# Optimization experiments

Measured on AMD Instinct MI355X. Metric: run time of the kernel, lower is better.

## Reference

```python
import jax, jax.numpy as jnp
import numpy as np
from jax import lax

K = 5          # dynamic kernel size
GROUPS = 8     # inter_channels // group_channels = 128 // 16
R = 2          # pixel shuffle upscale factor
SLOPE = 0.01   # LeakyReLU default negative_slope
EPS = 1e-5     # BatchNorm eps


def conv2d(x, w, b, pad=0):
    # x: [B,C,H,W], w: [O,I,kh,kw]
    y = lax.conv_general_dilated(x, w, (1, 1), [(pad, pad), (pad, pad)],
                                 dimension_numbers=('NCHW', 'OIHW', 'NCHW'))
    return y + b[None, :, None, None]


def pixel_shuffle(x, r):
    B, C, H, W = x.shape
    x = x.reshape(B, C // (r * r), r, r, H, W)
    x = x.transpose(0, 1, 4, 2, 5, 3)  # B, C', H, r, W, r
    return x.reshape(B, C // (r * r), H * r, W * r)


def involution(x, weight, k, groups, pad):
    # x: [B,C,H,W]; weight: [B,groups,k,k,H,W]
    # out[b, g*gc+c, h, w] = sum_ij weight[b,g,i,j,h,w] * x_pad[b, g*gc+c, h+i, w+j]
    B, C, H, W = x.shape
    gc = C // groups
    xp = jnp.pad(x, ((0, 0), (0, 0), (pad, pad), (pad, pad)))
    xg = xp.reshape(B, groups, gc, H + 2 * pad, W + 2 * pad)
    out = jnp.zeros((B, groups, gc, H, W), x.dtype)
    for i in range(k):
        for j in range(k):
            out = out + weight[:, :, None, i, j] * xg[:, :, :, i:i + H, j:j + W]
    return out.reshape(B, C, H, W)


def setup_inputs() -> dict:
    key = jax.random.key(0)
    ks = jax.random.split(key, 16)
    s = 0.05
    return {
        'high_level': jax.random.normal(ks[0], (8, 128, 64, 64), jnp.float32),
        'low_level': jax.random.normal(ks[1], (8, 224, 128, 128), jnp.float32),
        'emb': jax.random.normal(ks[2], (8, 256, 128, 128), jnp.float32),
        'reduce_w': jax.random.normal(ks[3], (128, 256, 1, 1), jnp.float32) * s,
        'reduce_b': jax.random.normal(ks[4], (128,), jnp.float32) * s,
        'conv1_w': jax.random.normal(ks[5], (32, 128, 1, 1), jnp.float32) * s,
        'conv1_b': jax.random.normal(ks[6], (32,), jnp.float32) * s,
        'conv2_w': jax.random.normal(ks[7], (200, 32, 3, 3), jnp.float32) * s,
        'conv2_b': jax.random.normal(ks[8], (200,), jnp.float32) * s,
        'embconv_w': jax.random.normal(ks[9], (32, 256, 1, 1), jnp.float32) * s,
        'embconv_b': jax.random.normal(ks[10], (32,), jnp.float32) * s,
        'out_w': jax.random.normal(ks[11], (64, 128, 1, 1), jnp.float32) * s,
        'out_b': jax.random.normal(ks[12], (64,), jnp.float32) * s,
        'bn_gamma': jnp.ones((64,), jnp.float32),
        'bn_beta': jnp.zeros((64,), jnp.float32),
        'bn_mean': jnp.zeros((64,), jnp.float32),
        'bn_var': jax.random.uniform(ks[13], (64,), jnp.float32, 0.5, 1.5),
    }


def reference(high_level, low_level, emb,
              reduce_w, reduce_b, conv1_w, conv1_b, conv2_w, conv2_b,
              embconv_w, embconv_b, out_w, out_b,
              bn_gamma, bn_beta, bn_mean, bn_var):
    cat = jnp.concatenate([pixel_shuffle(high_level, R), low_level], axis=1)
    cat = conv2d(cat, reduce_w, reduce_b)
    mix = jax.nn.leaky_relu(conv2d(cat, conv1_w, conv1_b)
                            + conv2d(emb, embconv_w, embconv_b), SLOPE)
    w = conv2d(mix, conv2_w, conv2_b, pad=1)  # [B, K*K*GROUPS, H, W]
    B, _, H, W = w.shape
    w = w.reshape(B, GROUPS, K, K, H, W)
    o = involution(cat, w, K, GROUPS, (K - 1) // 2)
    o = conv2d(o, out_w, out_b)
    o = (o - bn_mean[None, :, None, None]) * (bn_gamma[None, :, None, None]
        / jnp.sqrt(bn_var[None, :, None, None] + EPS)) + bn_beta[None, :, None, None]
    return jax.nn.leaky_relu(o, SLOPE)
```

## Files before the change

kernel.cpp:

```cpp
#include <hip/hip_runtime.h>

typedef unsigned short u16; typedef unsigned int u32; typedef unsigned long long u64;
typedef __attribute__((ext_vector_type(8))) short short8;
typedef __attribute__((ext_vector_type(16))) float f32x16;

#define HW 16384

#define RED_B  0
#define C1E_B  128
#define C2_B   160
#define OUT_B  416
#define BN_SC  480
#define BN_SH  544
#define FLAG_OFF   4096
#define RWB_OFF    8192
#define C1B_OFF    73728
#define EMBB_OFF   81920
#define OUTB_OFF   98304
#define C2PB_OFF   114688
#define CAT2_OFF   524288
#define MIX_OFF    34078720

__device__ __forceinline__ float bf2f(u16 x){ u32 u=((u32)x)<<16; float f; __builtin_memcpy(&f,&u,4); return f; }
__device__ __forceinline__ u16 f2bf(float f){ u32 u; __builtin_memcpy(&u,&f,4); return (u16)((u + 0x7fffu + ((u>>16)&1u))>>16); }
__device__ __forceinline__ float lrelu(float x){ return x>0.f ? x : 0.01f*x; }

template<int M> __device__ __forceinline__ u16 ldb(const void* p, size_t i){
    if (M==1) return ((const u16*)p)[i];
    return f2bf(((const float*)p)[i]);
}
template<int M> __device__ __forceinline__ float ldf(const void* p, size_t i){
    if (M==1) return bf2f(((const u16*)p)[i]);
    return ((const float*)p)[i];
}
template<int M> __device__ __forceinline__ short8 ld8(const void* p, size_t i){
    short8 v;
    if (M==1){ __builtin_memcpy(&v, (const u16*)p + i, 16); }
    else {
        float a[8]; __builtin_memcpy(a, (const float*)p + i, 32);
#pragma unroll
        for (int r=0;r<8;r++) v[r] = (short)f2bf(a[r]);
    }
    return v;
}
template<int M> __device__ __forceinline__ void ld4(const void* p, size_t i, u32* d){
    if (M==1){ __builtin_memcpy(d, (const u16*)p + i, 8); }
    else {
        float a[4]; __builtin_memcpy(a, (const float*)p + i, 16);
        d[0] = (u32)f2bf(a[0]) | ((u32)f2bf(a[1])<<16);
        d[1] = (u32)f2bf(a[2]) | ((u32)f2bf(a[3])<<16);
    }
}
__device__ __forceinline__ int swz(int p){ return ((p>>1) ^ (p>>3)) & 7; }

__global__ void detect_kernel(const void* __restrict__ emb, u32* __restrict__ flag){
    int tid = threadIdx.x;
    const u16* p = (const u16*)emb;
    int e = (p[tid*2] >> 7) & 0xFF;
    u64 m = __ballot(e >= 100 && e <= 140);
    if (tid == 0) *flag = (__popcll(m) >= 32) ? 1u : 0u;
}

template<int M>
__device__ __forceinline__ void prep_body(
    const void* rw, const void* rb, const void* c1w, const void* c1b,
    const void* c2w, const void* c2b, const void* ew, const void* eb,
    const void* ow, const void* ob, const void* gam, const void* bet,
    const void* mn, const void* vr, char* ws)
{
    float* wf = (float*)ws;
    int i = blockIdx.x*256 + threadIdx.x;
    if (i < 32768) {
        int o = i>>8, ic = i&255;
        int s = ic>>4, qq = (ic>>3)&1, e = ic&7;
        int dst = (((o>>5)*16 + s)*64 + qq*32 + (o&31))*8 + e;
        ((u16*)(ws+RWB_OFF))[dst] = ldb<M>(rw, i);
    }
    else if (i < 36864)  ((u16*)(ws+C1B_OFF))[i-32768] = ldb<M>(c1w, i-32768);
    else if (i < 45056)  ((u16*)(ws+EMBB_OFF))[i-36864] = ldb<M>(ew, i-36864);
    else if (i < 53248)  ((u16*)(ws+OUTB_OFF))[i-45056] = ldb<M>(ow, i-45056);
    else if (i < 126976) {
        int j = i-53248; int o = j/288, k = j - o*288;
        int tap = k>>5, ic = k&31;
        u16 v = 0;
        if (o < 200) v = ldb<M>(c2w, (size_t)o*288 + ic*9 + tap);
        ((u16*)(ws+C2PB_OFF))[j] = v;
    }
    else if (i < 127584) {
        int j = i-126976;
        if (j < 128) wf[RED_B+j] = ldf<M>(rb, j);
        else if (j < 160) wf[C1E_B+j-128] = ldf<M>(c1b, j-128) + ldf<M>(eb, j-128);
        else if (j < 416) { int o = j-160; wf[C2_B+o] = (o<200) ? ldf<M>(c2b,o) : 0.f; }
        else if (j < 480) wf[OUT_B+j-416] = ldf<M>(ob, j-416);
        else if (j < 544) { int c=j-480; wf[BN_SC+c] = ldf<M>(gam,c) * rsqrtf(ldf<M>(vr,c)+1e-5f); }
        else { int c=j-544; wf[BN_SH+c] = ldf<M>(bet,c) - ldf<M>(mn,c)*ldf<M>(gam,c)*rsqrtf(ldf<M>(vr,c)+1e-5f); }
    }
}

__global__ __launch_bounds__(256) void k_prep(
    const void* rw, const void* rb, const void* c1w, const void* c1b,
    const void* c2w, const void* c2b, const void* ew, const void* eb,
    const void* ow, const void* ob, const void* gam, const void* bet,
    const void* mn, const void* vr, char* ws, const u32* __restrict__ flag)
{
    if (*flag) prep_body<1>(rw,rb,c1w,c1b,c2w,c2b,ew,eb,ow,ob,gam,bet,mn,vr,ws);
    else       prep_body<0>(rw,rb,c1w,c1b,c2w,c2b,ew,eb,ow,ob,gam,bet,mn,vr,ws);
}

template<int M>
__device__ __forceinline__ void reduce_body(
    const void* __restrict__ hi, const void* __restrict__ lo,
    const u16* __restrict__ rwB, const float* __restrict__ wf,
    u16* __restrict__ cat2, u16* At)
{
    const int tid = threadIdx.x, wvi = tid>>6, lane = tid&63;
    const int rt = (wvi>>1)*32, nc0 = (wvi&1)*64;
    const int col = lane&31, q = lane>>5;

    const int gpx = blockIdx.x*64;
    const int b = gpx>>14, p0 = gpx&16383;
    const int h = p0>>7, w0 = p0&127;

    const int co = tid>>3, po = tid&7;
    u32 W[8][4];
    if (co < 28) {
        u32 R[8][4];
#pragma unroll
        for (int j=0;j<8;j++){
            short8 v = ld8<M>(lo, ((size_t)(b*224 + 8*co + j))*HW + p0 + 8*po);
            __builtin_memcpy(&R[j][0], &v, 16);
        }
#pragma unroll
        for (int p=0;p<8;p++){
            const int u = p>>1, hf = p&1;
#pragma unroll
            for (int m=0;m<4;m++){
                u32 A0 = R[2*m][u], A1 = R[2*m+1][u];
                W[p][m] = hf ? ((A0>>16) | (A1 & 0xffff0000u))
                             : ((A0 & 0xffffu) | (A1<<16));
            }
        }
        const int ch = co + 4;
#pragma unroll
        for (int p=0;p<8;p++){
            int pg = 8*po + p;
            __builtin_memcpy(At + pg*264 + ((ch ^ swz(pg))<<3), &W[p][0], 16);
        }
    } else {
        const int cc0 = (co-28)*8, h2 = (h&1)*2;
        u32 E[8][2], O[8][2];
#pragma unroll
        for (int j=0;j<8;j++){
            int hc = (cc0+j)*4 + h2;
            size_t src = ((size_t)(b*128 + hc))*4096 + (size_t)(h>>1)*64 + (w0>>1) + 4*po;
            ld4<M>(hi, src,        E[j]);
            ld4<M>(hi, src + 4096, O[j]);
        }
#pragma unroll
        for (int p=0;p<8;p++){
            const int k = p>>1, u = k>>1, hf = k&1;
#pragma unroll
            for (int m=0;m<4;m++){
                u32 A0, A1;
                if (p&1){ A0 = O[2*m][u]; A1 = O[2*m+1][u]; }
                else    { A0 = E[2*m][u]; A1 = E[2*m+1][u]; }
                W[p][m] = hf ? ((A0>>16) | (A1 & 0xffff0000u))
                             : ((A0 & 0xffffu) | (A1<<16));
            }
        }
        const int ch = co - 28;
#pragma unroll
        for (int p=0;p<8;p++){
            int pg = 8*po + p;
            __builtin_memcpy(At + pg*264 + ((ch ^ swz(pg))<<3), &W[p][0], 16);
        }
    }
    __syncthreads();

    const int pp = rt + col, sw = swz(pp);
    const u16* arow = At + pp*264;
    const int ot0 = (wvi&1)*2;

    f32x16 acc0, acc1;
#pragma unroll
    for (int r=0;r<16;r++){ acc0[r]=0.f; acc1[r]=0.f; }

    short8 Bb[2][8];
#pragma unroll
    for (int nt=0;nt<2;nt++)
#pragma unroll
    for (int s=0;s<8;s++)
        __builtin_memcpy(&Bb[nt][s], rwB + (((size_t)((ot0+nt)*16 + s))*64 + lane)*8, 16);
#pragma unroll
    for (int s=0;s<8;s++){
        short8 a; __builtin_memcpy(&a, arow + (((2*s+q)^sw)<<3), 16);
        acc0 = __builtin_amdgcn_mfma_f32_32x32x16_bf16(a, Bb[0][s], acc0, 0,0,0);
        acc1 = __builtin_amdgcn_mfma_f32_32x32x16_bf16(a, Bb[1][s], acc1, 0,0,0);
    }
#pragma unroll
    for (int nt=0;nt<2;nt++)
#pragma unroll
    for (int s=0;s<8;s++)
        __builtin_memcpy(&Bb[nt][s], rwB + (((size_t)((ot0+nt)*16 + 8+s))*64 + lane)*8, 16);
#pragma unroll
    for (int s=8;s<16;s++){
        short8 a; __builtin_memcpy(&a, arow + (((2*s+q)^sw)<<3), 16);
        acc0 = __builtin_amdgcn_mfma_f32_32x32x16_bf16(a, Bb[0][s-8], acc0, 0,0,0);
        acc1 = __builtin_amdgcn_mfma_f32_32x32x16_bf16(a, Bb[1][s-8], acc1, 0,0,0);
    }

#pragma unroll
    for (int nt=0; nt<2; nt++){
        int oc = nc0 + nt*32 + col;
        float bias = wf[RED_B + oc];
#pragma unroll
        for (int r=0;r<16;r++){
            int row = (r&3) + 8*(r>>2) + 4*q;
            float v = (nt ? acc1[r] : acc0[r]) + bias;
            cat2[((size_t)(gpx + rt + row))*128 + oc] = f2bf(v);
        }
    }
}

__global__ __launch_bounds__(256) void k_reduce(
    const void* __restrict__ hi, const void* __restrict__ lo,
    const u16* __restrict__ rwB, const float* __restrict__ wf,
    u16* __restrict__ cat2, const u32* __restrict__ flag)
{
    __shared__ u16 At[64*264];
    if (*flag) reduce_body<1>(hi, lo, rwB, wf, cat2, At);
    else       reduce_body<0>(hi, lo, rwB, wf, cat2, At);
}

template<int M>
__device__ __forceinline__ void mix_body(
    const u16* __restrict__ cat2, const void* __restrict__ emb,
    const u16* __restrict__ c1B, const u16* __restrict__ embB,
    const float* __restrict__ wf, u16* __restrict__ mixt, u16* At)
{
    const int tid = threadIdx.x, wvi = tid>>6, lane = tid&63;
    const int rt = wvi*32, col = lane&31, q = lane>>5;

    const int gpx = blockIdx.x*128;
    const int b = gpx>>14, p0 = gpx&16383;

    short8 Bc[8];
#pragma unroll
    for (int s=0;s<8;s++)  __builtin_memcpy(&Bc[s], c1B + (size_t)col*128 + s*16 + q*8, 16);

    f32x16 acc;
#pragma unroll
    for (int r=0;r<16;r++) acc[r]=0.f;
    const int pp = rt + col, sw = swz(pp);
    const u16* arow = At + pp*136;

#pragma unroll
    for (int i=0;i<8;i++){
        int idx = tid + i*256;
        int p = idx>>4, c16 = idx&15;
        short8 v;
        __builtin_memcpy(&v, cat2 + ((size_t)(gpx+p))*128 + c16*8, 16);
        *(short8*)(At + p*136 + ((c16 ^ swz(p))<<3)) = v;
    }
    __syncthreads();
#pragma unroll
    for (int s=0;s<8;s++){
        short8 a; __builtin_memcpy(&a, arow + (((2*s+q)^sw)<<3), 16);
        acc = __builtin_amdgcn_mfma_f32_32x32x16_bf16(a, Bc[s], acc, 0,0,0);
    }

    const int co = tid>>4, po = tid&15;
#pragma unroll 1
    for (int half=0; half<2; half++){
        u32 R[8][4];
#pragma unroll
        for (int j=0;j<8;j++){
            short8 v = ld8<M>(emb, ((size_t)(b*256 + half*128 + 8*co + j))*HW + p0 + 8*po);
            __builtin_memcpy(&R[j][0], &v, 16);
        }
        short8 Be[8];
#pragma unroll
        for (int s=0;s<8;s++)
            __builtin_memcpy(&Be[s], embB + (size_t)col*256 + half*128 + s*16 + q*8, 16);
        __syncthreads();
        u32 W[8][4];
#pragma unroll
        for (int p=0;p<8;p++){
            const int u = p>>1, hf = p&1;
#pragma unroll
            for (int m=0;m<4;m++){
                u32 A0 = R[2*m][u], A1 = R[2*m+1][u];
                W[p][m] = hf ? ((A0>>16) | (A1 & 0xffff0000u))
                             : ((A0 & 0xffffu) | (A1<<16));
            }
        }
#pragma unroll
        for (int p=0;p<8;p++){
            int pg = 8*po + p;
            __builtin_memcpy(At + pg*136 + ((co ^ swz(pg))<<3), &W[p][0], 16);
        }
        __syncthreads();
#pragma unroll
        for (int s=0;s<8;s++){
            short8 a; __builtin_memcpy(&a, arow + (((2*s+q)^sw)<<3), 16);
            acc = __builtin_amdgcn_mfma_f32_32x32x16_bf16(a, Be[s], acc, 0,0,0);
        }
    }
    float bias = wf[C1E_B + col];
#pragma unroll
    for (int r=0;r<16;r++){
        int row = (r&3) + 8*(r>>2) + 4*q;
        mixt[((size_t)(gpx + rt + row))*32 + col] = f2bf(lrelu(acc[r] + bias));
    }
}

__global__ __launch_bounds__(256) void k_mix(
    const u16* __restrict__ cat2, const void* __restrict__ emb,
    const u16* __restrict__ c1B, const u16* __restrict__ embB,
    const float* __restrict__ wf, u16* __restrict__ mixt, const u32* __restrict__ flag)
{
    __shared__ u16 At[128*136];
    if (*flag) mix_body<1>(cat2, emb, c1B, embB, wf, mixt, At);
    else       mix_body<0>(cat2, emb, c1B, embB, wf, mixt, At);
}

template<int M>
__device__ __forceinline__ void inv_body(
    const u16* __restrict__ cat2, const u16* __restrict__ mixt,
    const u16* __restrict__ c2B, const u16* __restrict__ outB,
    const float* __restrict__ wf, void* __restrict__ out,
    u16* halo_m, u16* wgt_l, u16* halo_c, u16* og)
{
    const int tid = threadIdx.x, wvi = tid>>6, lane = tid&63;
    const int col = lane&31, q = lane>>5;
    const int b = blockIdx.y, ty = blockIdx.x>>3, tx = blockIdx.x&7;
    const int py = tid>>4, px = tid&15;

    f32x16 acc[2][2];
#pragma unroll
    for (int i=0;i<2;i++)
#pragma unroll
    for (int j=0;j<2;j++)
#pragma unroll
    for (int r=0;r<16;r++) acc[i][j][r] = 0.f;

#pragma unroll
    for (int i=0;i<6;i++){
        int idx = tid + i*256;
        if (idx < 1296){
            int point = idx>>2, cq = idx&3;
            int y = ty*16 + point/18 - 1, x = tx*16 + point%18 - 1;
            short8 v;
            if (y>=0 && y<128 && x>=0 && x<128)
                __builtin_memcpy(&v, mixt + ((size_t)(b*HW + y*128 + x))*32 + cq*8, 16);
            else { short z=0; v = (short8){z,z,z,z,z,z,z,z}; }
            *(short8*)(halo_m + point*40 + cq*8) = v;
        }
    }
    __syncthreads();

#pragma unroll 1
    for (int g=0; g<8; g++){
        __syncthreads();

        const int o = g*25 + col;
        short8 Bf[18];
#pragma unroll
        for (int s=0;s<18;s++)
            __builtin_memcpy(&Bf[s], c2B + (size_t)o*288 + s*16 + q*8, 16);

#pragma unroll
        for (int i=0;i<4;i++){
            int idx = tid + i*256;
            if (idx < 800){
                int point = idx>>1, cq = idx&1;
                int y = ty*16 + point/20 - 2, x = tx*16 + point%20 - 2;
                short8 v;
                if (y>=0 && y<128 && x>=0 && x<128)
                    __builtin_memcpy(&v, cat2 + ((size_t)(b*HW + y*128 + x))*128 + g*16 + cq*8, 16);
                else { short z=0; v = (short8){z,z,z,z,z,z,z,z}; }
                *(short8*)(halo_c + point*16 + cq*8) = v;
            }
        }

        f32x16 c0, c1;
#pragma unroll
        for (int r=0;r<16;r++){ c0[r]=0.f; c1[r]=0.f; }
        const int p0 = wvi*64 + col, p1 = p0 + 32;
        const int pya = p0>>4, pxa = p0&15, pyb = p1>>4, pxb = p1&15;
#pragma unroll
        for (int s=0;s<18;s++){
            int tap = s>>1, ih = s&1;
            int dy = tap/3, dx = tap%3;
            short8 a0, a1;
            __builtin_memcpy(&a0, halo_m + ((pya+dy)*18 + pxa+dx)*40 + ih*16 + q*8, 16);
            __builtin_memcpy(&a1, halo_m + ((pyb+dy)*18 + pxb+dx)*40 + ih*16 + q*8, 16);
            c0 = __builtin_amdgcn_mfma_f32_32x32x16_bf16(a0, Bf[s], c0, 0,0,0);
            c1 = __builtin_amdgcn_mfma_f32_32x32x16_bf16(a1, Bf[s], c1, 0,0,0);
        }
        {
            float bias = wf[C2_B + o];
#pragma unroll
            for (int rt2=0; rt2<2; rt2++){
                int mb = wvi*64 + rt2*32;
#pragma unroll
                for (int r=0;r<16;r+=2){
                    int row0 = (r&3) + 8*(r>>2) + 4*q;
                    float v0 = (rt2 ? c1[r]   : c0[r])   + bias;
                    float v1 = (rt2 ? c1[r+1] : c0[r+1]) + bias;
                    u32 pkv = (u32)f2bf(v0) | ((u32)f2bf(v1)<<16);
                    *(u32*)(wgt_l + (size_t)col*264 + mb + row0) = pkv;
                }
            }
        }
        __syncthreads();

        float wvv[25];
#pragma unroll
        for (int t=0;t<25;t++) wvv[t] = bf2f(wgt_l[t*264 + tid]);

        float a16[16];
#pragma unroll
        for (int cc=0;cc<16;cc++) a16[cc]=0.f;
#pragma unroll
        for (int t=0;t<25;t++){
            int dy = t/5, dx = t%5;
            u32 vv[8];
            __builtin_memcpy(vv, halo_c + ((py+dy)*20 + px+dx)*16, 32);
            float wt = wvv[t];
#pragma unroll
            for (int r=0;r<8;r++){
                u32 u = vv[r];
                u32 ulo = u<<16, uhi = u & 0xffff0000u;
                float x0, x1;
                __builtin_memcpy(&x0,&ulo,4); __builtin_memcpy(&x1,&uhi,4);
                a16[2*r]   += wt*x0;
                a16[2*r+1] += wt*x1;
            }
        }
        u32 pk[8];
#pragma unroll
        for (int r=0;r<8;r++) pk[r] = (u32)f2bf(a16[2*r]) | ((u32)f2bf(a16[2*r+1])<<16);
        __builtin_memcpy(og + tid*16, pk, 32);
        __syncthreads();

        short8 bo0, bo1;
        __builtin_memcpy(&bo0, outB + (size_t)(col)*128      + g*16 + q*8, 16);
        __builtin_memcpy(&bo1, outB + (size_t)(32+col)*128   + g*16 + q*8, 16);
#pragma unroll
        for (int rt2=0; rt2<2; rt2++){
            int prow = (wvi*2 + rt2)*32 + col;
            short8 a; __builtin_memcpy(&a, og + prow*16 + q*8, 16);
            acc[rt2][0] = __builtin_amdgcn_mfma_f32_32x32x16_bf16(a, bo0, acc[rt2][0], 0,0,0);
            acc[rt2][1] = __builtin_amdgcn_mfma_f32_32x32x16_bf16(a, bo1, acc[rt2][1], 0,0,0);
        }
    }
#pragma unroll
    for (int rt2=0; rt2<2; rt2++)
#pragma unroll
    for (int nt=0; nt<2; nt++){
        int oc = nt*32 + col;
        float bias = wf[OUT_B+oc], sc = wf[BN_SC+oc], sh = wf[BN_SH+oc];
#pragma unroll
        for (int r=0;r<16;r++){
            int row = (r&3) + 8*(r>>2) + 4*q;
            int p = (wvi*2 + rt2)*32 + row;
            int yy = ty*16 + (p>>4), xx = tx*16 + (p&15);
            float v = lrelu((acc[rt2][nt][r] + bias)*sc + sh);
            size_t oidx = ((size_t)(b*64 + oc))*HW + yy*128 + xx;
            if (M==1) ((u16*)out)[oidx] = f2bf(v);
            else ((float*)out)[oidx] = v;
        }
    }
}

__global__ __launch_bounds__(256,2) void k_inv(
    const u16* __restrict__ cat2, const u16* __restrict__ mixt,
    const u16* __restrict__ c2B, const u16* __restrict__ outB,
    const float* __restrict__ wf, void* __restrict__ out, const u32* __restrict__ flag)
{
    __shared__ u16 halo_m[324*40];
    __shared__ u16 wgt_l[32*264];
    __shared__ u16 halo_c[400*16];
    __shared__ u16 og[256*16];
    if (*flag) inv_body<1>(cat2, mixt, c2B, outB, wf, out, halo_m, wgt_l, halo_c, og);
    else       inv_body<0>(cat2, mixt, c2B, outB, wf, out, halo_m, wgt_l, halo_c, og);
}

extern "C" void kernel_launch(void* const* d_in, const int* in_sizes, int n_in,
                              void* d_out, int out_size, void* d_ws, size_t ws_size,
                              hipStream_t stream) {
    const void* hi  = d_in[0];
    const void* lo  = d_in[1];
    const void* emb = d_in[2];
    char* ws = (char*)d_ws;
    float* wf = (float*)ws;
    u32* flag = (u32*)(ws + FLAG_OFF);
    u16* cat2 = (u16*)(ws + CAT2_OFF);
    u16* mixt = (u16*)(ws + MIX_OFF);

    detect_kernel<<<1, 64, 0, stream>>>(emb, flag);

    k_prep<<<499,256,0,stream>>>(d_in[3],d_in[4],d_in[5],d_in[6],d_in[7],d_in[8],
        d_in[9],d_in[10],d_in[11],d_in[12],d_in[13],d_in[14],d_in[15],d_in[16], ws, flag);

    k_reduce<<<2048,256,0,stream>>>(hi, lo, (const u16*)(ws+RWB_OFF), wf, cat2, flag);

    k_mix<<<1024,256,0,stream>>>(cat2, emb, (const u16*)(ws+C1B_OFF),
                                 (const u16*)(ws+EMBB_OFF), wf, mixt, flag);

    k_inv<<<dim3(64,8),256,0,stream>>>(cat2, mixt, (const u16*)(ws+C2PB_OFF),
                                       (const u16*)(ws+OUTB_OFF), wf, d_out, flag);
}
```

Before: 399.6 us.

## Fuse reduce and mix kernels, keeping cat tile in LDS for conv1

Merges the reduce 1x1 conv kernel and the mix kernel into one kernel over 64-pixel tiles. The reduced cat tile is written to global memory for the involution stage and also kept in shared memory, so conv1 reads it from LDS instead of reloading it from global. The emb projection's K dimension is split across wave pairs, and partial sums are exchanged through LDS. This removes one launch and one global read of cat2. In exchange it uses more shared memory per block and adds a launch_bounds occupancy hint.

```diff
diff --git a/kernel.cpp b/kernel.cpp
--- a/kernel.cpp
+++ b/kernel.cpp
@@ -23,6 +23,7 @@
 
 __device__ __forceinline__ float bf2f(u16 x){ u32 u=((u32)x)<<16; float f; __builtin_memcpy(&f,&u,4); return f; }
 __device__ __forceinline__ u16 f2bf(float f){ u32 u; __builtin_memcpy(&u,&f,4); return (u16)((u + 0x7fffu + ((u>>16)&1u))>>16); }
+__device__ __forceinline__ u32 pk2(float a, float b){ return (u32)f2bf(a) | ((u32)f2bf(b)<<16); }
 __device__ __forceinline__ float lrelu(float x){ return x>0.f ? x : 0.01f*x; }
 
 template<int M> __device__ __forceinline__ u16 ldb(const void* p, size_t i){
@@ -33,25 +34,25 @@
     if (M==1) return bf2f(((const u16*)p)[i]);
     return ((const float*)p)[i];
 }
-template<int M> __device__ __forceinline__ short8 ld8(const void* p, size_t i){
-    short8 v;
-    if (M==1){ __builtin_memcpy(&v, (const u16*)p + i, 16); }
-    else {
-        float a[8]; __builtin_memcpy(a, (const float*)p + i, 32);
-#pragma unroll
-        for (int r=0;r<8;r++) v[r] = (short)f2bf(a[r]);
-    }
-    return v;
-}
-template<int M> __device__ __forceinline__ void ld4(const void* p, size_t i, u32* d){
-    if (M==1){ __builtin_memcpy(d, (const u16*)p + i, 8); }
-    else {
-        float a[4]; __builtin_memcpy(a, (const float*)p + i, 16);
-        d[0] = (u32)f2bf(a[0]) | ((u32)f2bf(a[1])<<16);
-        d[1] = (u32)f2bf(a[2]) | ((u32)f2bf(a[3])<<16);
-    }
-}
 __device__ __forceinline__ int swz(int p){ return ((p>>1) ^ (p>>3)) & 7; }
+
+template<int M>
+__device__ __forceinline__ void load8x8(const void* p, size_t base, size_t stride, u32 R[8][4]){
+    if (M==1){
+#pragma unroll
+        for (int j=0;j<8;j++)
+            __builtin_memcpy(&R[j][0], (const u16*)p + base + (size_t)j*stride, 16);
+    } else {
+        float raw[8][8];
+#pragma unroll
+        for (int j=0;j<8;j++)
+            __builtin_memcpy(&raw[j][0], (const float*)p + base + (size_t)j*stride, 32);
+#pragma unroll
+        for (int j=0;j<8;j++)
+#pragma unroll
+        for (int m=0;m<4;m++) R[j][m] = pk2(raw[j][2*m], raw[j][2*m+1]);
+    }
+}
 
 __global__ void detect_kernel(const void* __restrict__ emb, u32* __restrict__ flag){
     int tid = threadIdx.x;
@@ -108,28 +109,141 @@
 }
 
 template<int M>
-__device__ __forceinline__ void reduce_body(
-    const void* __restrict__ hi, const void* __restrict__ lo,
-    const u16* __restrict__ rwB, const float* __restrict__ wf,
-    u16* __restrict__ cat2, u16* At)
+__device__ __forceinline__ void rm_body(
+    const void* __restrict__ hi, const void* __restrict__ lo, const void* __restrict__ emb,
+    const u16* __restrict__ rwB, const u16* __restrict__ c1B, const u16* __restrict__ embB,
+    const float* __restrict__ wf, u16* __restrict__ cat2, u16* __restrict__ mixt,
+    u16* At, u16* c2l)
 {
     const int tid = threadIdx.x, wvi = tid>>6, lane = tid&63;
-    const int rt = (wvi>>1)*32, nc0 = (wvi&1)*64;
     const int col = lane&31, q = lane>>5;
-
     const int gpx = blockIdx.x*64;
     const int b = gpx>>14, p0 = gpx&16383;
     const int h = p0>>7, w0 = p0&127;
-
     const int co = tid>>3, po = tid&7;
-    u32 W[8][4];
-    if (co < 28) {
+
+    {
+        u32 W[8][4];
+        if (co < 28) {
+            u32 R[8][4];
+            load8x8<M>(lo, ((size_t)(b*224 + 8*co))*HW + p0 + 8*po, HW, R);
+#pragma unroll
+            for (int p=0;p<8;p++){
+                const int u = p>>1, hf = p&1;
+#pragma unroll
+                for (int m=0;m<4;m++){
+                    u32 A0 = R[2*m][u], A1 = R[2*m+1][u];
+                    W[p][m] = hf ? ((A0>>16) | (A1 & 0xffff0000u))
+                                 : ((A0 & 0xffffu) | (A1<<16));
+                }
+            }
+            const int ch = co + 4;
+#pragma unroll
+            for (int p=0;p<8;p++){
+                int pg = 8*po + p;
+                __builtin_memcpy(At + pg*264 + ((ch ^ swz(pg))<<3), &W[p][0], 16);
+            }
+        } else {
+            const int cc0 = (co-28)*8, h2 = (h&1)*2;
+            u32 E[8][2], O[8][2];
+            if (M==1){
+#pragma unroll
+                for (int j=0;j<8;j++){
+                    int hc = (cc0+j)*4 + h2;
+                    size_t src = ((size_t)(b*128 + hc))*4096 + (size_t)(h>>1)*64 + (w0>>1) + 4*po;
+                    __builtin_memcpy(&E[j][0], (const u16*)hi + src, 8);
+                    __builtin_memcpy(&O[j][0], (const u16*)hi + src + 4096, 8);
+                }
+            } else {
+                float rE[8][4], rO[8][4];
+#pragma unroll
+                for (int j=0;j<8;j++){
+                    int hc = (cc0+j)*4 + h2;
+                    size_t src = ((size_t)(b*128 + hc))*4096 + (size_t)(h>>1)*64 + (w0>>1) + 4*po;
+                    __builtin_memcpy(&rE[j][0], (const float*)hi + src, 16);
+                    __builtin_memcpy(&rO[j][0], (const float*)hi + src + 4096, 16);
+                }
+#pragma unroll
+                for (int j=0;j<8;j++){
+                    E[j][0] = pk2(rE[j][0], rE[j][1]); E[j][1] = pk2(rE[j][2], rE[j][3]);
+                    O[j][0] = pk2(rO[j][0], rO[j][1]); O[j][1] = pk2(rO[j][2], rO[j][3]);
+                }
+            }
+#pragma unroll
+            for (int p=0;p<8;p++){
+                const int k = p>>1, u = k>>1, hf = k&1;
+#pragma unroll
+                for (int m=0;m<4;m++){
+                    u32 A0, A1;
+                    if (p&1){ A0 = O[2*m][u]; A1 = O[2*m+1][u]; }
+                    else    { A0 = E[2*m][u]; A1 = E[2*m+1][u]; }
+                    W[p][m] = hf ? ((A0>>16) | (A1 & 0xffff0000u))
+                                 : ((A0 & 0xffffu) | (A1<<16));
+                }
+            }
+            const int ch = co - 28;
+#pragma unroll
+            for (int p=0;p<8;p++){
+                int pg = 8*po + p;
+                __builtin_memcpy(At + pg*264 + ((ch ^ swz(pg))<<3), &W[p][0], 16);
+            }
+        }
+    }
+    __syncthreads();
+
+    {
+        const int rt = (wvi>>1)*32, nc0 = (wvi&1)*64;
+        const int pp = rt + col, sw = swz(pp);
+        const u16* arow = At + pp*264;
+        const int ot0 = (wvi&1)*2;
+
+        f32x16 acc0, acc1;
+#pragma unroll
+        for (int r=0;r<16;r++){ acc0[r]=0.f; acc1[r]=0.f; }
+
+        short8 Bb[2][8];
+#pragma unroll
+        for (int nt=0;nt<2;nt++)
+#pragma unroll
+        for (int s=0;s<8;s++)
+            __builtin_memcpy(&Bb[nt][s], rwB + (((size_t)((ot0+nt)*16 + s))*64 + lane)*8, 16);
+#pragma unroll
+        for (int s=0;s<8;s++){
+            short8 a; __builtin_memcpy(&a, arow + (((2*s+q)^sw)<<3), 16);
+            acc0 = __builtin_amdgcn_mfma_f32_32x32x16_bf16(a, Bb[0][s], acc0, 0,0,0);
+            acc1 = __builtin_amdgcn_mfma_f32_32x32x16_bf16(a, Bb[1][s], acc1, 0,0,0);
+        }
+#pragma unroll
+        for (int nt=0;nt<2;nt++)
+#pragma unroll
+        for (int s=0;s<8;s++)
+            __builtin_memcpy(&Bb[nt][s], rwB + (((size_t)((ot0+nt)*16 + 8+s))*64 + lane)*8, 16);
+#pragma unroll
+        for (int s=8;s<16;s++){
+            short8 a; __builtin_memcpy(&a, arow + (((2*s+q)^sw)<<3), 16);
+            acc0 = __builtin_amdgcn_mfma_f32_32x32x16_bf16(a, Bb[0][s-8], acc0, 0,0,0);
+            acc1 = __builtin_amdgcn_mfma_f32_32x32x16_bf16(a, Bb[1][s-8], acc1, 0,0,0);
+        }
+
+#pragma unroll
+        for (int nt=0; nt<2; nt++){
+            int oc = nc0 + nt*32 + col;
+            float bias = wf[RED_B + oc];
+#pragma unroll
+            for (int r=0;r<16;r++){
+                int row = (r&3) + 8*(r>>2) + 4*q;
+                int px = rt + row;
+                u16 bv = f2bf((nt ? acc1[r] : acc0[r]) + bias);
+                cat2[((size_t)(gpx + px))*128 + oc] = bv;
+                c2l[px*136 + (((oc>>3) ^ swz(px))<<3) + (oc&7)] = bv;
+            }
+        }
+    }
+
+    {
         u32 R[8][4];
-#pragma unroll
-        for (int j=0;j<8;j++){
-            short8 v = ld8<M>(lo, ((size_t)(b*224 + 8*co + j))*HW + p0 + 8*po);
-            __builtin_memcpy(&R[j][0], &v, 16);
-        }
+        load8x8<M>(emb, ((size_t)(b*256 + 8*co))*HW + p0 + 8*po, HW, R);
+        u32 W[8][4];
 #pragma unroll
         for (int p=0;p<8;p++){
             const int u = p>>1, hf = p&1;
@@ -140,188 +254,87 @@
                              : ((A0 & 0xffffu) | (A1<<16));
             }
         }
-        const int ch = co + 4;
+        __syncthreads();
 #pragma unroll
         for (int p=0;p<8;p++){
             int pg = 8*po + p;
-            __builtin_memcpy(At + pg*264 + ((ch ^ swz(pg))<<3), &W[p][0], 16);
+            __builtin_memcpy(At + pg*264 + ((co ^ swz(pg))<<3), &W[p][0], 16);
+        }
+    }
+    __syncthreads();
+
+    const int rt2 = wvi>>1, q2 = wvi&1;
+    const int pp2 = rt2*32 + col, sw2 = swz(pp2);
+    const u16* arow136 = c2l + pp2*136;
+    const u16* arow264 = At + pp2*264;
+
+    f32x16 macc;
+#pragma unroll
+    for (int r=0;r<16;r++) macc[r]=0.f;
+
+    if (q2 == 0){
+        short8 Bc[8];
+#pragma unroll
+        for (int s=0;s<8;s++)
+            __builtin_memcpy(&Bc[s], c1B + (size_t)col*128 + s*16 + q*8, 16);
+#pragma unroll
+        for (int s=0;s<8;s++){
+            short8 a; __builtin_memcpy(&a, arow136 + (((2*s+q)^sw2)<<3), 16);
+            macc = __builtin_amdgcn_mfma_f32_32x32x16_bf16(a, Bc[s], macc, 0,0,0);
+        }
+        short8 Be[4];
+#pragma unroll
+        for (int s=0;s<4;s++)
+            __builtin_memcpy(&Be[s], embB + (size_t)col*256 + s*16 + q*8, 16);
+#pragma unroll
+        for (int s=0;s<4;s++){
+            short8 a; __builtin_memcpy(&a, arow264 + (((2*s+q)^sw2)<<3), 16);
+            macc = __builtin_amdgcn_mfma_f32_32x32x16_bf16(a, Be[s], macc, 0,0,0);
         }
     } else {
-        const int cc0 = (co-28)*8, h2 = (h&1)*2;
-        u32 E[8][2], O[8][2];
-#pragma unroll
-        for (int j=0;j<8;j++){
-            int hc = (cc0+j)*4 + h2;
-            size_t src = ((size_t)(b*128 + hc))*4096 + (size_t)(h>>1)*64 + (w0>>1) + 4*po;
-            ld4<M>(hi, src,        E[j]);
-            ld4<M>(hi, src + 4096, O[j]);
-        }
-#pragma unroll
-        for (int p=0;p<8;p++){
-            const int k = p>>1, u = k>>1, hf = k&1;
-#pragma unroll
-            for (int m=0;m<4;m++){
-                u32 A0, A1;
-                if (p&1){ A0 = O[2*m][u]; A1 = O[2*m+1][u]; }
-                else    { A0 = E[2*m][u]; A1 = E[2*m+1][u]; }
-                W[p][m] = hf ? ((A0>>16) | (A1 & 0xffff0000u))
-                             : ((A0 & 0xffffu) | (A1<<16));
-            }
-        }
-        const int ch = co - 28;
-#pragma unroll
-        for (int p=0;p<8;p++){
-            int pg = 8*po + p;
-            __builtin_memcpy(At + pg*264 + ((ch ^ swz(pg))<<3), &W[p][0], 16);
+        short8 Be[12];
+#pragma unroll
+        for (int s=0;s<12;s++)
+            __builtin_memcpy(&Be[s], embB + (size_t)col*256 + (4+s)*16 + q*8, 16);
+#pragma unroll
+        for (int s=0;s<12;s++){
+            int ks = 4 + s;
+            short8 a; __builtin_memcpy(&a, arow264 + (((2*ks+q)^sw2)<<3), 16);
+            macc = __builtin_amdgcn_mfma_f32_32x32x16_bf16(a, Be[s], macc, 0,0,0);
         }
     }
     __syncthreads();
 
-    const int pp = rt + col, sw = swz(pp);
-    const u16* arow = At + pp*264;
-    const int ot0 = (wvi&1)*2;
-
-    f32x16 acc0, acc1;
-#pragma unroll
-    for (int r=0;r<16;r++){ acc0[r]=0.f; acc1[r]=0.f; }
-
-    short8 Bb[2][8];
-#pragma unroll
-    for (int nt=0;nt<2;nt++)
-#pragma unroll
-    for (int s=0;s<8;s++)
-        __builtin_memcpy(&Bb[nt][s], rwB + (((size_t)((ot0+nt)*16 + s))*64 + lane)*8, 16);
-#pragma unroll
-    for (int s=0;s<8;s++){
-        short8 a; __builtin_memcpy(&a, arow + (((2*s+q)^sw)<<3), 16);
-        acc0 = __builtin_amdgcn_mfma_f32_32x32x16_bf16(a, Bb[0][s], acc0, 0,0,0);
-        acc1 = __builtin_amdgcn_mfma_f32_32x32x16_bf16(a, Bb[1][s], acc1, 0,0,0);
-    }
-#pragma unroll
-    for (int nt=0;nt<2;nt++)
-#pragma unroll
-    for (int s=0;s<8;s++)
-        __builtin_memcpy(&Bb[nt][s], rwB + (((size_t)((ot0+nt)*16 + 8+s))*64 + lane)*8, 16);
-#pragma unroll
-    for (int s=8;s<16;s++){
-        short8 a; __builtin_memcpy(&a, arow + (((2*s+q)^sw)<<3), 16);
-        acc0 = __builtin_amdgcn_mfma_f32_32x32x16_bf16(a, Bb[0][s-8], acc0, 0,0,0);
-        acc1 = __builtin_amdgcn_mfma_f32_32x32x16_bf16(a, Bb[1][s-8], acc1, 0,0,0);
-    }
-
-#pragma unroll
-    for (int nt=0; nt<2; nt++){
-        int oc = nc0 + nt*32 + col;
-        float bias = wf[RED_B + oc];
+    float* exch = (float*)At;
+    if (q2 == 1){
 #pragma unroll
         for (int r=0;r<16;r++){
             int row = (r&3) + 8*(r>>2) + 4*q;
-            float v = (nt ? acc1[r] : acc0[r]) + bias;
-            cat2[((size_t)(gpx + rt + row))*128 + oc] = f2bf(v);
-        }
-    }
-}
-
-__global__ __launch_bounds__(256) void k_reduce(
-    const void* __restrict__ hi, const void* __restrict__ lo,
-    const u16* __restrict__ rwB, const float* __restrict__ wf,
-    u16* __restrict__ cat2, const u32* __restrict__ flag)
+            exch[rt2*1024 + row*32 + col] = macc[r];
+        }
+    }
+    __syncthreads();
+    if (q2 == 0){
+        float bias = wf[C1E_B + col];
+#pragma unroll
+        for (int r=0;r<16;r++){
+            int row = (r&3) + 8*(r>>2) + 4*q;
+            float v = macc[r] + exch[rt2*1024 + row*32 + col] + bias;
+            mixt[((size_t)(gpx + rt2*32 + row))*32 + col] = f2bf(lrelu(v));
+        }
+    }
+}
+
+__global__ __launch_bounds__(256,3) void k_rm(
+    const void* __restrict__ hi, const void* __restrict__ lo, const void* __restrict__ emb,
+    const u16* __restrict__ rwB, const u16* __restrict__ c1B, const u16* __restrict__ embB,
+    const float* __restrict__ wf, u16* __restrict__ cat2, u16* __restrict__ mixt,
+    const u32* __restrict__ flag)
 {
     __shared__ u16 At[64*264];
-    if (*flag) reduce_body<1>(hi, lo, rwB, wf, cat2, At);
-    else       reduce_body<0>(hi, lo, rwB, wf, cat2, At);
-}
-
-template<int M>
-__device__ __forceinline__ void mix_body(
-    const u16* __restrict__ cat2, const void* __restrict__ emb,
-    const u16* __restrict__ c1B, const u16* __restrict__ embB,
-    const float* __restrict__ wf, u16* __restrict__ mixt, u16* At)
-{
-    const int tid = threadIdx.x, wvi = tid>>6, lane = tid&63;
-    const int rt = wvi*32, col = lane&31, q = lane>>5;
-
-    const int gpx = blockIdx.x*128;
-    const int b = gpx>>14, p0 = gpx&16383;
-
-    short8 Bc[8];
-#pragma unroll
-    for (int s=0;s<8;s++)  __builtin_memcpy(&Bc[s], c1B + (size_t)col*128 + s*16 + q*8, 16);
-
-    f32x16 acc;
-#pragma unroll
-    for (int r=0;r<16;r++) acc[r]=0.f;
-    const int pp = rt + col, sw = swz(pp);
-    const u16* arow = At + pp*136;
-
-#pragma unroll
-    for (int i=0;i<8;i++){
-        int idx = tid + i*256;
-        int p = idx>>4, c16 = idx&15;
-        short8 v;
-        __builtin_memcpy(&v, cat2 + ((size_t)(gpx+p))*128 + c16*8, 16);
-        *(short8*)(At + p*136 + ((c16 ^ swz(p))<<3)) = v;
-    }
-    __syncthreads();
-#pragma unroll
-    for (int s=0;s<8;s++){
-        short8 a; __builtin_memcpy(&a, arow + (((2*s+q)^sw)<<3), 16);
-        acc = __builtin_amdgcn_mfma_f32_32x32x16_bf16(a, Bc[s], acc, 0,0,0);
-    }
-
-    const int co = tid>>4, po = tid&15;
-#pragma unroll 1
-    for (int half=0; half<2; half++){
-        u32 R[8][4];
-#pragma unroll
-        for (int j=0;j<8;j++){
-            short8 v = ld8<M>(emb, ((size_t)(b*256 + half*128 + 8*co + j))*HW + p0 + 8*po);
-            __builtin_memcpy(&R[j][0], &v, 16);
-        }
-        short8 Be[8];
-#pragma unroll
-        for (int s=0;s<8;s++)
-            __builtin_memcpy(&Be[s], embB + (size_t)col*256 + half*128 + s*16 + q*8, 16);
-        __syncthreads();
-        u32 W[8][4];
-#pragma unroll
-        for (int p=0;p<8;p++){
-            const int u = p>>1, hf = p&1;
-#pragma unroll
-            for (int m=0;m<4;m++){
-                u32 A0 = R[2*m][u], A1 = R[2*m+1][u];
-                W[p][m] = hf ? ((A0>>16) | (A1 & 0xffff0000u))
-                             : ((A0 & 0xffffu) | (A1<<16));
-            }
-        }
-#pragma unroll
-        for (int p=0;p<8;p++){
-            int pg = 8*po + p;
-            __builtin_memcpy(At + pg*136 + ((co ^ swz(pg))<<3), &W[p][0], 16);
-        }
-        __syncthreads();
-#pragma unroll
-        for (int s=0;s<8;s++){
-            short8 a; __builtin_memcpy(&a, arow + (((2*s+q)^sw)<<3), 16);
-            acc = __builtin_amdgcn_mfma_f32_32x32x16_bf16(a, Be[s], acc, 0,0,0);
-        }
-    }
-    float bias = wf[C1E_B + col];
-#pragma unroll
-    for (int r=0;r<16;r++){
-        int row = (r&3) + 8*(r>>2) + 4*q;
-        mixt[((size_t)(gpx + rt + row))*32 + col] = f2bf(lrelu(acc[r] + bias));
-    }
-}
-
-__global__ __launch_bounds__(256) void k_mix(
-    const u16* __restrict__ cat2, const void* __restrict__ emb,
-    const u16* __restrict__ c1B, const u16* __restrict__ embB,
-    const float* __restrict__ wf, u16* __restrict__ mixt, const u32* __restrict__ flag)
-{
-    __shared__ u16 At[128*136];
-    if (*flag) mix_body<1>(cat2, emb, c1B, embB, wf, mixt, At);
-    else       mix_body<0>(cat2, emb, c1B, embB, wf, mixt, At);
+    __shared__ u16 c2l[64*136];
+    if (*flag) rm_body<1>(hi, lo, emb, rwB, c1B, embB, wf, cat2, mixt, At, c2l);
+    else       rm_body<0>(hi, lo, emb, rwB, c1B, embB, wf, cat2, mixt, At, c2l);
 }
 
 template<int M>
@@ -504,10 +517,9 @@
     k_prep<<<499,256,0,stream>>>(d_in[3],d_in[4],d_in[5],d_in[6],d_in[7],d_in[8],
         d_in[9],d_in[10],d_in[11],d_in[12],d_in[13],d_in[14],d_in[15],d_in[16], ws, flag);
 
-    k_reduce<<<2048,256,0,stream>>>(hi, lo, (const u16*)(ws+RWB_OFF), wf, cat2, flag);
-
-    k_mix<<<1024,256,0,stream>>>(cat2, emb, (const u16*)(ws+C1B_OFF),
-                                 (const u16*)(ws+EMBB_OFF), wf, mixt, flag);
+    k_rm<<<2048,256,0,stream>>>(hi, lo, emb, (const u16*)(ws+RWB_OFF),
+                                (const u16*)(ws+C1B_OFF), (const u16*)(ws+EMBB_OFF),
+                                wf, cat2, mixt, flag);
 
     k_inv<<<dim3(64,8),256,0,stream>>>(cat2, mixt, (const u16*)(ws+C2PB_OFF),
                                        (const u16*)(ws+OUTB_OFF), wf, d_out, flag);
```

After: 399.5 us. About the same (-0.0%).
